# Kernel optimization log

Measured on AMD Instinct MI355X. Metric: run time of the kernel, lower is better.

## Reference

```python
import jax, jax.numpy as jnp
import numpy as np
from jax import lax

NUM_SEG = 64
EPS = 1e-12

def conv2d(x, w, b=None):
    y = lax.conv_general_dilated(x, w, (1, 1), 'SAME', dimension_numbers=('NCHW', 'OIHW', 'NCHW'))
    if b is not None:
        y = y + b[None, :, None, None]
    return y

def layer_norm_chw(x):
    # LayerNorm over (C,H,W) per sample, no affine
    mu = x.mean(axis=(1, 2, 3), keepdims=True)
    var = jnp.mean((x - mu) ** 2, axis=(1, 2, 3), keepdims=True)
    return (x - mu) / jnp.sqrt(var + EPS)

def spade(x, sem_rs, w_sh, b_sh, w_g, b_g, w_be, b_be):
    xn = layer_norm_chw(x)
    h = jax.nn.relu(conv2d(sem_rs, w_sh, b_sh))
    gamma = conv2d(h, w_g, b_g)
    beta = conv2d(h, w_be, b_be)
    return xn * (1.0 + gamma) + beta

def painted_semantic_map(f_sem, segmap):
    # f_sem: [B,C,Hp,Wp] float; segmap: [B,Hi,Wi] int
    B, C, Hp, Wp = f_sem.shape
    _, Hi, Wi = segmap.shape
    # torch nearest interpolate: src = floor(dst * in/out)
    rows = (jnp.arange(Hp) * Hi) // Hp
    cols = (jnp.arange(Wp) * Wi) // Wp
    seg_small = segmap[:, rows[:, None], cols[None, :]]  # [B,Hp,Wp]
    flat_feat = f_sem.transpose(0, 2, 3, 1).reshape(-1, C)  # [B*Hp*Wp, C]
    bidx = jnp.repeat(jnp.arange(B), Hp * Wp)
    gid = bidx * NUM_SEG + jnp.clip(seg_small.reshape(-1), 0, NUM_SEG - 1)
    sums = jax.ops.segment_sum(flat_feat, gid, num_segments=B * NUM_SEG)
    cnts = jax.ops.segment_sum(jnp.ones((flat_feat.shape[0],), flat_feat.dtype), gid, num_segments=B * NUM_SEG)
    # scatter_mean + nan_to_num: empty segments -> 0
    avg = jnp.where(cnts[:, None] > 0, sums / jnp.maximum(cnts, 1.0)[:, None], 0.0)
    pid = jnp.repeat(jnp.arange(B), Hi * Wi) * NUM_SEG + jnp.clip(segmap.reshape(-1), 0, NUM_SEG - 1)
    return avg[pid].reshape(B, Hi, Wi, C).transpose(0, 3, 1, 2)  # [B,C,Hi,Wi]

def setup_inputs() -> dict:
    key = jax.random.key(0)
    ks = jax.random.split(key, 32)
    B, Cm, Cs, Hp, Wp, Hi, Wi, Hm = 2, 1536, 384, 32, 32, 448, 448, 128
    d = {}
    d['x_main'] = jax.random.normal(ks[0], (B, Cm, Hp, Wp), jnp.float32)
    d['f_semantic'] = jax.random.normal(ks[1], (B, Cs, Hp, Wp), jnp.float32)
    s = 0.02
    d['w_sh0'] = jax.random.normal(ks[2], (Hm, Cs, 3, 3), jnp.float32) * s
    d['b_sh0'] = jax.random.normal(ks[3], (Hm,), jnp.float32) * s
    d['w_g0'] = jax.random.normal(ks[4], (Cm, Hm, 3, 3), jnp.float32) * s
    d['b_g0'] = jax.random.normal(ks[5], (Cm,), jnp.float32) * s
    d['w_be0'] = jax.random.normal(ks[6], (Cm, Hm, 3, 3), jnp.float32) * s
    d['b_be0'] = jax.random.normal(ks[7], (Cm,), jnp.float32) * s
    d['w_sh1'] = jax.random.normal(ks[8], (Hm, Cs, 3, 3), jnp.float32) * s
    d['b_sh1'] = jax.random.normal(ks[9], (Hm,), jnp.float32) * s
    d['w_g1'] = jax.random.normal(ks[10], (8, Hm, 3, 3), jnp.float32) * s
    d['b_g1'] = jax.random.normal(ks[11], (8,), jnp.float32) * s
    d['w_be1'] = jax.random.normal(ks[12], (8, Hm, 3, 3), jnp.float32) * s
    d['b_be1'] = jax.random.normal(ks[13], (8,), jnp.float32) * s
    d['w_sh2'] = jax.random.normal(ks[14], (Hm, Cs, 3, 3), jnp.float32) * s
    d['b_sh2'] = jax.random.normal(ks[15], (Hm,), jnp.float32) * s
    d['w_g2'] = jax.random.normal(ks[16], (16, Hm, 3, 3), jnp.float32) * s
    d['b_g2'] = jax.random.normal(ks[17], (16,), jnp.float32) * s
    d['w_be2'] = jax.random.normal(ks[18], (16, Hm, 3, 3), jnp.float32) * s
    d['b_be2'] = jax.random.normal(ks[19], (16,), jnp.float32) * s
    d['w_c0'] = jax.random.normal(ks[20], (8, Cm, 1, 1), jnp.float32) * s
    d['bias0'] = jax.random.normal(ks[21], (8,), jnp.float32) * s
    d['w_c1'] = jax.random.normal(ks[22], (16, 8, 1, 1), jnp.float32) * s
    d['bias1'] = jax.random.normal(ks[23], (16,), jnp.float32) * s
    d['w_c2'] = jax.random.normal(ks[24], (1, 16, 1, 1), jnp.float32) * s
    d['bias2'] = jax.random.normal(ks[25], (1,), jnp.float32) * s
    d['segmap'] = jax.random.randint(ks[26], (B, Hi, Wi), 0, NUM_SEG, jnp.int32)
    return d

def reference(x_main, f_semantic, w_sh0, b_sh0, w_g0, b_g0, w_be0, b_be0,
              w_sh1, b_sh1, w_g1, b_g1, w_be1, b_be1,
              w_sh2, b_sh2, w_g2, b_g2, w_be2, b_be2,
              w_c0, bias0, w_c1, bias1, w_c2, bias2, segmap):
    B, Cm, Hp, Wp = x_main.shape
    pm = painted_semantic_map(f_semantic, segmap)  # [B,Cs,Hi,Wi]
    # bilinear (align_corners=False) resize to main-path resolution; identical at all 3 SPADE layers
    sem_rs = jax.image.resize(pm, (B, pm.shape[1], Hp, Wp), method='bilinear')
    h = spade(x_main, sem_rs, w_sh0, b_sh0, w_g0, b_g0, w_be0, b_be0)
    h = jax.nn.softplus(conv2d(h, w_c0) + bias0[None, :, None, None])
    h = spade(h, sem_rs, w_sh1, b_sh1, w_g1, b_g1, w_be1, b_be1)
    h = jax.nn.softplus(conv2d(h, w_c1) + bias1[None, :, None, None])
    h = spade(h, sem_rs, w_sh2, b_sh2, w_g2, b_g2, w_be2, b_be2)
    h = jax.nn.softplus(conv2d(h, w_c2) + bias2[None, :, None, None])
    return h
```

## Files before the change

kernel.cpp:

```cpp
#include <hip/hip_runtime.h>
#include <hip/hip_bf16.h>

#define DEV __device__ __forceinline__

constexpr int B = 2;
constexpr int CM = 1536;
constexpr int CS = 384;
constexpr int HP = 32, WP = 32, P = 1024;
constexpr int HI = 448, WI = 448;
constexpr int HM = 128;
constexpr int NSEG = 64;

constexpr size_t OFF_AVG  = 0;
constexpr size_t OFF_SEMT = 49152;
constexpr size_t OFF_HSHT = 835584;
constexpr size_t OFF_OUT0 = 1622016;
constexpr size_t OFF_P6   = 4767744;
constexpr size_t OFF_H1A  = 5160960;
constexpr size_t OFF_OUT1 = 5177344;
constexpr size_t OFF_H2A  = 5193728;
constexpr size_t OFF_OUT2 = 5226496;
constexpr size_t OFF_STATS= 5259264;
constexpr size_t OFF_PACK = 5259280;

constexpr size_t PK0 = 0;
constexpr size_t PK1 = 1327104;
constexpr size_t PK2 = 4866048;
constexpr size_t PK3 = 4902912;
constexpr int    PK_CHUNKS = 617472;

typedef __attribute__((ext_vector_type(8))) short s16x8;
typedef __attribute__((ext_vector_type(4))) float f32x4;

DEV float softplus_f(float x) {
    return fmaxf(x, 0.f) + log1pf(expf(-fabsf(x)));
}
DEV ushort f2bf(float f) {
    union { float f; unsigned u; } x; x.f = f;
    unsigned r = x.u + 0x7fffu + ((x.u >> 16) & 1u);
    return (ushort)(r >> 16);
}
DEV float bf2f(ushort u) {
    union { unsigned u; float f; } x; x.u = ((unsigned)u) << 16;
    return x.f;
}

__global__ __launch_bounds__(256) void k_seg_avg(const float* __restrict__ f_sem,
                                                 const int* __restrict__ segmap,
                                                 float* __restrict__ ws) {
    int b = blockIdx.y;
    int c0 = blockIdx.x * 8;
    __shared__ int   segs[P];
    __shared__ float sums[NSEG][9];
    __shared__ float cnt[NSEG];
    int t = threadIdx.x;
    for (int i = t; i < NSEG * 9; i += 256) (&sums[0][0])[i] = 0.f;
    if (t < NSEG) cnt[t] = 0.f;
    __syncthreads();
    for (int p = t; p < P; p += 256) {
        int i = p >> 5, j = p & 31;
        int s = segmap[(b * HI + i * 14) * WI + j * 14];
        s = min(max(s, 0), NSEG - 1);
        segs[p] = s;
        atomicAdd(&cnt[s], 1.f);
    }
    __syncthreads();
    #pragma unroll
    for (int ch = 0; ch < 8; ++ch) {
        const float* fp = f_sem + ((size_t)b * CS + c0 + ch) * P;
        #pragma unroll
        for (int pb = 0; pb < 4; ++pb) {
            int p = pb * 256 + t;
            float v = fp[p];
            atomicAdd(&sums[segs[p]][ch], v);
        }
    }
    __syncthreads();
    for (int i = t; i < NSEG * 8; i += 256) {
        int s = i >> 3, ch = i & 7;
        float cv = cnt[s];
        ws[OFF_AVG + ((size_t)(b * NSEG + s)) * CS + c0 + ch] =
            cv > 0.f ? sums[s][ch] / cv : 0.f;
    }
}

__global__ __launch_bounds__(256) void k_paint(const int* __restrict__ segmap,
                                               float* __restrict__ ws) {
    int oxt = blockIdx.x, oy = blockIdx.y, b = blockIdx.z;
    int ox0 = oxt * 8;
    __shared__ float WbT[8][65];
    __shared__ float norm[8];
    int t = threadIdx.x;
    for (int i = t; i < 8 * 65; i += 256) (&WbT[0][0])[i] = 0.f;
    __syncthreads();

    float cy = 14.f * oy + 6.5f;
    int y0 = 14 * oy - 7;
    int x0 = 14 * ox0 - 7;
    for (int k = t; k < 28 * 126; k += 256) {
        int r = k / 126, cix = k % 126;
        int jy = y0 + r, jx = x0 + cix;
        if (jy < 0 || jy >= HI || jx < 0 || jx >= WI) continue;
        float wy = 1.f - fabsf(cy - (float)jy) * (1.f / 14.f);
        int s = segmap[(b * HI + jy) * WI + jx];
        s = min(max(s, 0), NSEG - 1);
        int oxhi = (jx + 7) / 14;
        #pragma unroll
        for (int d = 0; d < 2; ++d) {
            int ox = oxhi - d;
            if (ox < ox0 || ox >= ox0 + 8) continue;
            float wx = 1.f - fabsf(14.f * ox + 6.5f - (float)jx) * (1.f / 14.f);
            if (wx > 0.f) atomicAdd(&WbT[ox - ox0][s], wy * wx);
        }
    }
    __syncthreads();
    if (t < 8) {
        float sm = 0.f;
        #pragma unroll
        for (int s = 0; s < NSEG; ++s) sm += WbT[t][s];
        norm[t] = 1.f / sm;
    }
    __syncthreads();

    const float* ap0 = ws + OFF_AVG + (size_t)b * NSEG * CS;
    for (int c = t; c < CS; c += 256) {
        float acc[8] = {};
        const float* ap = ap0 + c;
        #pragma unroll
        for (int s = 0; s < NSEG; ++s) {
            float a = ap[(size_t)s * CS];
            #pragma unroll
            for (int ox = 0; ox < 8; ++ox) acc[ox] += WbT[ox][s] * a;
        }
        #pragma unroll
        for (int ox = 0; ox < 8; ++ox) {
            int op = oy * 32 + ox0 + ox;
            ws[OFF_SEMT + ((size_t)b * P + op) * CS + c] = acc[ox] * norm[ox];
        }
    }
}

__global__ __launch_bounds__(256) void k_ln0_stats(const float* __restrict__ x,
                                                   float* __restrict__ stats) {
    int b = blockIdx.y;
    const float4* xp = (const float4*)(x + (size_t)b * CM * P);
    int n4 = CM * P / 4;
    float s = 0.f, q = 0.f;
    for (int i = blockIdx.x * 256 + threadIdx.x; i < n4; i += 64 * 256) {
        float4 v = xp[i];
        s += v.x + v.y + v.z + v.w;
        q += v.x * v.x + v.y * v.y + v.z * v.z + v.w * v.w;
    }
    for (int o = 32; o > 0; o >>= 1) { s += __shfl_down(s, o); q += __shfl_down(q, o); }
    __shared__ float ls[4], lq[4];
    int w = threadIdx.x >> 6;
    if ((threadIdx.x & 63) == 0) { ls[w] = s; lq[w] = q; }
    __syncthreads();
    if (threadIdx.x == 0) {
        atomicAdd(&stats[b * 2],     ls[0] + ls[1] + ls[2] + ls[3]);
        atomicAdd(&stats[b * 2 + 1], lq[0] + lq[1] + lq[2] + lq[3]);
    }
}

__global__ __launch_bounds__(256) void k_wpack(
    const float* __restrict__ w_sh0, const float* __restrict__ w_sh1, const float* __restrict__ w_sh2,
    const float* __restrict__ w_g0,  const float* __restrict__ w_be0,
    const float* __restrict__ w_g1,  const float* __restrict__ w_be1,
    const float* __restrict__ w_g2,  const float* __restrict__ w_be2,
    ushort* __restrict__ packU)
{
    for (int c8 = blockIdx.x * 256 + threadIdx.x; c8 < PK_CHUNKS; c8 += gridDim.x * 256) {
        size_t e = (size_t)c8 * 8;
        const float* s0 = nullptr;
        bool zero = false;
        if (e < PK1) {
            size_t r = e;
            int ci0 = (int)(r & 31), co2 = (int)((r >> 5) & 31);
            int tap = (int)((r >> 10) % 9);
            int kct = (int)((r / 9216) % 12), ct = (int)(r / 110592);
            int coG = ct * 32 + co2, sel = coG >> 7, cow = coG & 127;
            const float* wp = sel == 0 ? w_sh0 : (sel == 1 ? w_sh1 : w_sh2);
            s0 = &wp[((size_t)cow * CS + kct * 32 + ci0) * 9 + tap];
        } else if (e < PK2) {
            size_t r = e - PK1;
            int ci0 = (int)(r & 31), co2 = (int)((r >> 5) & 31);
            int tap = (int)((r >> 10) % 9);
            int kct = (int)((r / 9216) % 4), ct = (int)(r / 36864);
            int cog = ct * 16 + (co2 & 15);
            const float* wp = co2 < 16 ? w_g0 : w_be0;
            s0 = &wp[((size_t)cog * HM + kct * 32 + ci0) * 9 + tap];
        } else if (e < PK3) {
            size_t r = e - PK2;
            int ci0 = (int)(r & 31), co2 = (int)((r >> 5) & 31);
            int tap = (int)((r >> 10) % 9);
            int kct = (int)(r / 9216);
            zero = ((co2 & 15) >= 8);
            int cog = co2 & 7;
            const float* wp = co2 < 16 ? w_g1 : w_be1;
            if (!zero) s0 = &wp[((size_t)cog * HM + kct * 32 + ci0) * 9 + tap];
        } else {
            size_t r = e - PK3;
            int ci0 = (int)(r & 31), co2 = (int)((r >> 5) & 31);
            int tap = (int)((r >> 10) % 9);
            int kct = (int)(r / 9216);
            int cog = co2 & 15;
            const float* wp = co2 < 16 ? w_g2 : w_be2;
            s0 = &wp[((size_t)cog * HM + kct * 32 + ci0) * 9 + tap];
        }
        s16x8 o;
        #pragma unroll
        for (int i = 0; i < 8; ++i) {
            float v = zero ? 0.f : s0[(size_t)i * 9];
            o[i] = (short)f2bf(v);
        }
        *(s16x8*)&packU[e] = o;
    }
}

template<int MODE>
__global__ __launch_bounds__(256) void k_conv_mfma(
    const float* __restrict__ semT, const ushort* __restrict__ hshTin,
    const ushort* __restrict__ packW,
    const float* __restrict__ bb0, const float* __restrict__ bb1,
    const float* __restrict__ xsrc, const float* __restrict__ st, float Ninv,
    const float* __restrict__ wcf, const float* __restrict__ bcf,
    float* __restrict__ fout, float* __restrict__ statsOut,
    ushort* __restrict__ outH)
{
    constexpr int ROWS = (MODE == 0) ? 4 : 8;
    constexpr int NT   = ROWS / 2;
    constexpr int XR   = ROWS + 2;
    constexpr int KTOT = (MODE == 0) ? 12 : 4;
    constexpr int CBASE = (MODE == 2) ? 128 : (MODE == 3) ? 256 : 0;
    constexpr int NP = (MODE == 1) ? 1536 : (MODE == 2) ? 8 : 16;

    int pt = blockIdx.x, ctile = blockIdx.y;
    int zz = blockIdx.z;
    int b  = (MODE == 0) ? (zz % B) : zz;
    int ks = (MODE == 0) ? (zz / B) : 0;
    int t = threadIdx.x, l = t & 63, wv = t >> 6;
    int y0 = pt * ROWS;

    __shared__ __align__(16) ushort Wl[9][32][40];
    __shared__ __align__(16) ushort Xl[XR][34][40];

    f32x4 acc[2][NT] = {};

    for (int kc = 0; kc < 128; kc += 32) {
        __syncthreads();
        for (int j = t; j < XR * 34 * 4; j += 256) {
            int slot = j >> 2, part = j & 3;
            int r = slot / 34, c = slot % 34;
            int gy = y0 - 1 + r, gx = c - 1;
            s16x8 v = {};
            if (gy >= 0 && gy < HP && gx >= 0 && gx < WP) {
                int pix = gy * WP + gx;
                if constexpr (MODE == 0) {
                    const float4* sp = (const float4*)&semT[((size_t)b * P + pix) * CS + ks * 128 + kc + part * 8];
                    float4 x0 = sp[0], x1 = sp[1];
                    v[0] = (short)f2bf(x0.x); v[1] = (short)f2bf(x0.y);
                    v[2] = (short)f2bf(x0.z); v[3] = (short)f2bf(x0.w);
                    v[4] = (short)f2bf(x1.x); v[5] = (short)f2bf(x1.y);
                    v[6] = (short)f2bf(x1.z); v[7] = (short)f2bf(x1.w);
                } else {
                    v = *(const s16x8*)&hshTin[((size_t)b * P + pix) * 384 + CBASE + kc + part * 8];
                }
            }
            *(s16x8*)&Xl[r][c][part * 8] = v;
        }
        const ushort* wsrc = packW + (size_t)(ctile * KTOT + ks * 4 + (kc >> 5)) * 9216;
        for (int j = t; j < 1152; j += 256) {
            int tap = j >> 7, co2 = (j >> 2) & 31, part = j & 3;
            *(s16x8*)&Wl[tap][co2][part * 8] = *(const s16x8*)&wsrc[(size_t)j * 8];
        }
        __syncthreads();
        #pragma unroll
        for (int tap = 0; tap < 9; ++tap) {
            int dy = tap / 3, dx = tap % 3;
            s16x8 a0 = *(const s16x8*)&Wl[tap][l & 15][(l >> 4) * 8];
            s16x8 a1 = *(const s16x8*)&Wl[tap][16 + (l & 15)][(l >> 4) * 8];
            #pragma unroll
            for (int nt = 0; nt < NT; ++nt) {
                int q = wv * (16 * NT) + nt * 16 + (l & 15);
                int ry = (q >> 5) + dy, rx = (q & 31) + dx;
                s16x8 bf = *(const s16x8*)&Xl[ry][rx][(l >> 4) * 8];
                acc[0][nt] = __builtin_amdgcn_mfma_f32_16x16x32_bf16(a0, bf, acc[0][nt], 0, 0, 0);
                acc[1][nt] = __builtin_amdgcn_mfma_f32_16x16x32_bf16(a1, bf, acc[1][nt], 0, 0, 0);
            }
        }
    }

    if constexpr (MODE == 0) {
        __syncthreads();
        ushort (*T)[36] = (ushort(*)[36])(&Xl[0][0][0]);
        #pragma unroll
        for (int mt = 0; mt < 2; ++mt)
            #pragma unroll
            for (int nt = 0; nt < NT; ++nt)
                #pragma unroll
                for (int r = 0; r < 4; ++r) {
                    int m = mt * 16 + (l >> 4) * 4 + r;
                    int pl = wv * (16 * NT) + nt * 16 + (l & 15);
                    T[pl][m] = f2bf(acc[mt][nt][r]);
                }
        __syncthreads();
        int row = t >> 1, half = t & 1;
        ushort* dst = outH + ((size_t)((ks * B + b) * P) + pt * 128 + row) * 384 + ctile * 32 + half * 16;
        *(s16x8*)dst = *(const s16x8*)&T[row][half * 16];
    } else if constexpr (MODE == 1) {
        float mu = st[b * 2] * Ninv;
        float var = st[b * 2 + 1] * Ninv - mu * mu;
        float rs = rsqrtf(var + 1e-12f);
        __syncthreads();
        float (*WC)[17] = (float(*)[17])(&Wl[0][0][0]);
        if (t < 128) WC[t >> 4][t & 15] = wcf[(size_t)(t >> 4) * CM + ctile * 16 + (t & 15)];
        __syncthreads();
        float pacc[8][4] = {};
        #pragma unroll
        for (int nt = 0; nt < NT; ++nt)
            #pragma unroll
            for (int r = 0; r < 4; ++r) {
                int m = (l >> 4) * 4 + r;
                int cog = ctile * 16 + m;
                int px = pt * 256 + wv * 64 + nt * 16 + (l & 15);
                float gam = acc[0][nt][r] + bb0[cog];
                float bet = acc[1][nt][r] + bb1[cog];
                float xv = xsrc[((size_t)b * NP + cog) * P + px];
                float o0 = (xv - mu) * rs * (1.f + gam) + bet;
                #pragma unroll
                for (int o = 0; o < 8; ++o) pacc[o][nt] += WC[o][m] * o0;
            }
        #pragma unroll
        for (int o = 0; o < 8; ++o)
            #pragma unroll
            for (int nt = 0; nt < NT; ++nt) {
                float v = pacc[o][nt];
                v += __shfl_xor(v, 16);
                v += __shfl_xor(v, 32);
                if ((l >> 4) == 0)
                    fout[(((size_t)b * 96 + ctile) * 8 + o) * P + pt * 256 + wv * 64 + nt * 16 + l] = v;
            }
    } else if constexpr (MODE == 2) {
        float mu = st[b * 2] * Ninv;
        float var = st[b * 2 + 1] * Ninv - mu * mu;
        float rs = rsqrtf(var + 1e-12f);
        __syncthreads();
        float (*O1)[9] = (float(*)[9])(&Xl[0][0][0]);
        #pragma unroll
        for (int nt = 0; nt < NT; ++nt)
            #pragma unroll
            for (int r = 0; r < 4; ++r) {
                int m = (l >> 4) * 4 + r;
                if (m < 8) {
                    int pxl = wv * 64 + nt * 16 + (l & 15);
                    int px = pt * 256 + pxl;
                    float gam = acc[0][nt][r] + bb0[m];
                    float bet = acc[1][nt][r] + bb1[m];
                    float xv = xsrc[((size_t)b * NP + m) * P + px];
                    O1[pxl][m] = (xv - mu) * rs * (1.f + gam) + bet;
                }
            }
        __syncthreads();
        float vin[8];
        #pragma unroll
        for (int ci = 0; ci < 8; ++ci) vin[ci] = O1[t][ci];
        float s = 0.f, q = 0.f;
        #pragma unroll
        for (int o = 0; o < 16; ++o) {
            float a = bcf[o];
            #pragma unroll
            for (int ci = 0; ci < 8; ++ci) a += wcf[o * 8 + ci] * vin[ci];
            a = softplus_f(a);
            fout[((size_t)b * 16 + o) * P + pt * 256 + t] = a;
            s += a; q += a * a;
        }
        for (int o2 = 32; o2 > 0; o2 >>= 1) { s += __shfl_down(s, o2); q += __shfl_down(q, o2); }
        float* red = (float*)&Wl[0][0][0];
        if ((t & 63) == 0) { red[wv] = s; red[4 + wv] = q; }
        __syncthreads();
        if (t == 0) {
            atomicAdd(&statsOut[b * 2],     red[0] + red[1] + red[2] + red[3]);
            atomicAdd(&statsOut[b * 2 + 1], red[4] + red[5] + red[6] + red[7]);
        }
    } else {
        float mu = st[b * 2] * Ninv;
        float var = st[b * 2 + 1] * Ninv - mu * mu;
        float rs = rsqrtf(var + 1e-12f);
        __syncthreads();
        float (*O2)[17] = (float(*)[17])(&Xl[0][0][0]);
        #pragma unroll
        for (int nt = 0; nt < NT; ++nt)
            #pragma unroll
            for (int r = 0; r < 4; ++r) {
                int m = (l >> 4) * 4 + r;
                int pxl = wv * 64 + nt * 16 + (l & 15);
                int px = pt * 256 + pxl;
                float gam = acc[0][nt][r] + bb0[m];
                float bet = acc[1][nt][r] + bb1[m];
                float xv = xsrc[((size_t)b * NP + m) * P + px];
                O2[pxl][m] = (xv - mu) * rs * (1.f + gam) + bet;
            }
        __syncthreads();
        float a = bcf[0];
        #pragma unroll
        for (int ci = 0; ci < 16; ++ci) a += wcf[ci] * O2[t][ci];
        fout[(size_t)b * P + pt * 256 + t] = softplus_f(a);
    }
}

__global__ __launch_bounds__(256) void k_hsh_fin(const ushort* __restrict__ part,
                                                 const float* __restrict__ b0,
                                                 const float* __restrict__ b1,
                                                 const float* __restrict__ b2,
                                                 ushort* __restrict__ hsh) {
    int gid = blockIdx.x * 256 + threadIdx.x;
    int grp = gid % 48, pixg = gid / 48;
    int ch0 = grp * 8;
    size_t base = (size_t)pixg * 384 + ch0;
    s16x8 p0 = *(const s16x8*)&part[(size_t)0 * B * P * 384 + base];
    s16x8 p1 = *(const s16x8*)&part[(size_t)1 * B * P * 384 + base];
    s16x8 p2 = *(const s16x8*)&part[(size_t)2 * B * P * 384 + base];
    int sel = ch0 >> 7;
    const float* bp = sel == 0 ? b0 : (sel == 1 ? b1 : b2);
    int cb = ch0 & 127;
    s16x8 o;
    #pragma unroll
    for (int i = 0; i < 8; ++i) {
        float v = bf2f((ushort)p0[i]) + bf2f((ushort)p1[i]) + bf2f((ushort)p2[i]) + bp[cb + i];
        o[i] = (short)f2bf(fmaxf(v, 0.f));
    }
    *(s16x8*)&hsh[base] = o;
}

__global__ __launch_bounds__(256) void k_c1a_fin(const float* __restrict__ part,
                                                 const float* __restrict__ bias,
                                                 float* __restrict__ h1a,
                                                 float* __restrict__ stats) {
    int b = blockIdx.y, t = threadIdx.x;
    int idx = blockIdx.x * 256 + t;
    int o = idx >> 10, pix = idx & 1023;
    float v = 0.f;
    #pragma unroll 8
    for (int ct = 0; ct < 96; ++ct)
        v += part[(((size_t)b * 96 + ct) * 8 + o) * P + pix];
    v += bias[o];
    v = softplus_f(v);
    h1a[((size_t)b * 8 + o) * P + pix] = v;
    float s = v, q = v * v;
    for (int o2 = 32; o2 > 0; o2 >>= 1) { s += __shfl_down(s, o2); q += __shfl_down(q, o2); }
    __shared__ float ls[4], lq[4];
    int w = t >> 6;
    if ((t & 63) == 0) { ls[w] = s; lq[w] = q; }
    __syncthreads();
    if (t == 0) {
        atomicAdd(&stats[(B + b) * 2],     ls[0] + ls[1] + ls[2] + ls[3]);
        atomicAdd(&stats[(B + b) * 2 + 1], lq[0] + lq[1] + lq[2] + lq[3]);
    }
}

extern "C" void kernel_launch(void* const* d_in, const int* in_sizes, int n_in,
                              void* d_out, int out_size, void* d_ws, size_t ws_size,
                              hipStream_t stream) {
    const float* x_main = (const float*)d_in[0];
    const float* f_sem  = (const float*)d_in[1];
    const float* w_sh0 = (const float*)d_in[2];  const float* b_sh0 = (const float*)d_in[3];
    const float* w_g0  = (const float*)d_in[4];  const float* b_g0  = (const float*)d_in[5];
    const float* w_be0 = (const float*)d_in[6];  const float* b_be0 = (const float*)d_in[7];
    const float* w_sh1 = (const float*)d_in[8];  const float* b_sh1 = (const float*)d_in[9];
    const float* w_g1  = (const float*)d_in[10]; const float* b_g1  = (const float*)d_in[11];
    const float* w_be1 = (const float*)d_in[12]; const float* b_be1 = (const float*)d_in[13];
    const float* w_sh2 = (const float*)d_in[14]; const float* b_sh2 = (const float*)d_in[15];
    const float* w_g2  = (const float*)d_in[16]; const float* b_g2  = (const float*)d_in[17];
    const float* w_be2 = (const float*)d_in[18]; const float* b_be2 = (const float*)d_in[19];
    const float* w_c0  = (const float*)d_in[20]; const float* bias0 = (const float*)d_in[21];
    const float* w_c1  = (const float*)d_in[22]; const float* bias1 = (const float*)d_in[23];
    const float* w_c2  = (const float*)d_in[24]; const float* bias2 = (const float*)d_in[25];
    const int*   segmap = (const int*)d_in[26];

    float* ws = (float*)d_ws;
    float* out = (float*)d_out;
    float* stats = ws + OFF_STATS;
    ushort* hshU = (ushort*)(ws + OFF_HSHT);
    ushort* partU = (ushort*)(ws + OFF_OUT0);
    float*  partA = ws + OFF_OUT0;
    ushort* packU = (ushort*)(ws + OFF_PACK);

    hipMemsetAsync((void*)stats, 0, 16 * sizeof(float), stream);

    k_wpack<<<dim3(2412), 256, 0, stream>>>(w_sh0, w_sh1, w_sh2, w_g0, w_be0,
                                            w_g1, w_be1, w_g2, w_be2, packU);
    k_seg_avg<<<dim3(48, B), 256, 0, stream>>>(f_sem, segmap, ws);
    k_ln0_stats<<<dim3(64, B), 256, 0, stream>>>(x_main, stats);
    k_paint<<<dim3(4, 32, B), 256, 0, stream>>>(segmap, ws);

    k_conv_mfma<0><<<dim3(8, 12, 3 * B), 256, 0, stream>>>(
        ws + OFF_SEMT, nullptr, packU + PK0,
        nullptr, nullptr, nullptr, nullptr, 0.f,
        nullptr, nullptr, nullptr, nullptr, partU);
    k_hsh_fin<<<dim3(384), 256, 0, stream>>>(partU, b_sh0, b_sh1, b_sh2, hshU);

    k_conv_mfma<1><<<dim3(4, 96, B), 256, 0, stream>>>(
        nullptr, hshU, packU + PK1,
        b_g0, b_be0, x_main, stats, 1.f / (float)(CM * P),
        w_c0, nullptr, partA, nullptr, nullptr);
    k_c1a_fin<<<dim3(32, B), 256, 0, stream>>>(partA, bias0, ws + OFF_H1A, stats);

    k_conv_mfma<2><<<dim3(4, 1, B), 256, 0, stream>>>(
        nullptr, hshU, packU + PK2,
        b_g1, b_be1, ws + OFF_H1A, stats + 2 * B, 1.f / (float)(8 * P),
        w_c1, bias1, ws + OFF_H2A, stats + 4 * B, nullptr);

    k_conv_mfma<3><<<dim3(4, 1, B), 256, 0, stream>>>(
        nullptr, hshU, packU + PK3,
        b_g2, b_be2, ws + OFF_H2A, stats + 4 * B, 1.f / (float)(16 * P),
        w_c2, bias2, out, nullptr, nullptr);
}
```

Measured before the change: 306.4 us.

## Split paint into weight-table and GEMV kernels, emit bf16, coalesce weight packing

```diff
diff --git a/kernel.cpp b/kernel.cpp
--- a/kernel.cpp
+++ b/kernel.cpp
@@ -15,11 +15,9 @@
 constexpr size_t OFF_SEMT = 49152;
 constexpr size_t OFF_HSHT = 835584;
 constexpr size_t OFF_OUT0 = 1622016;
-constexpr size_t OFF_P6   = 4767744;
+constexpr size_t OFF_WTBL = 4767744;
 constexpr size_t OFF_H1A  = 5160960;
-constexpr size_t OFF_OUT1 = 5177344;
 constexpr size_t OFF_H2A  = 5193728;
-constexpr size_t OFF_OUT2 = 5226496;
 constexpr size_t OFF_STATS= 5259264;
 constexpr size_t OFF_PACK = 5259280;
 
@@ -27,7 +25,6 @@
 constexpr size_t PK1 = 1327104;
 constexpr size_t PK2 = 4866048;
 constexpr size_t PK3 = 4902912;
-constexpr int    PK_CHUNKS = 617472;
 
 typedef __attribute__((ext_vector_type(8))) short s16x8;
 typedef __attribute__((ext_vector_type(4))) float f32x4;
@@ -84,8 +81,8 @@
     }
 }
 
-__global__ __launch_bounds__(256) void k_paint(const int* __restrict__ segmap,
-                                               float* __restrict__ ws) {
+__global__ __launch_bounds__(256) void k_paint_w(const int* __restrict__ segmap,
+                                                 float* __restrict__ Wt) {
     int oxt = blockIdx.x, oy = blockIdx.y, b = blockIdx.z;
     int ox0 = oxt * 8;
     __shared__ float WbT[8][65];
@@ -121,22 +118,41 @@
         norm[t] = 1.f / sm;
     }
     __syncthreads();
-
-    const float* ap0 = ws + OFF_AVG + (size_t)b * NSEG * CS;
-    for (int c = t; c < CS; c += 256) {
-        float acc[8] = {};
-        const float* ap = ap0 + c;
-        #pragma unroll
-        for (int s = 0; s < NSEG; ++s) {
-            float a = ap[(size_t)s * CS];
-            #pragma unroll
-            for (int ox = 0; ox < 8; ++ox) acc[ox] += WbT[ox][s] * a;
-        }
-        #pragma unroll
-        for (int ox = 0; ox < 8; ++ox) {
-            int op = oy * 32 + ox0 + ox;
-            ws[OFF_SEMT + ((size_t)b * P + op) * CS + c] = acc[ox] * norm[ox];
-        }
+    for (int i = t; i < 8 * 64; i += 256) {
+        int ox = i >> 6, s = i & 63;
+        int op = oy * 32 + ox0 + ox;
+        Wt[((size_t)b * P + op) * 64 + s] = WbT[ox][s] * norm[ox];
+    }
+}
+
+__global__ __launch_bounds__(256) void k_paint_gemv(const float* __restrict__ Wt,
+                                                    const float* __restrict__ avg,
+                                                    ushort* __restrict__ semB) {
+    int pt = blockIdx.x, ctb = blockIdx.y, b = blockIdx.z;
+    __shared__ float WL[32][65];
+    __shared__ float AL[64][33];
+    int t = threadIdx.x;
+    for (int i = t; i < 2048; i += 256) {
+        int p = i >> 6, s = i & 63;
+        WL[p][s] = Wt[((size_t)b * P + pt * 32 + p) * 64 + s];
+    }
+    for (int i = t; i < 2048; i += 256) {
+        int s = i >> 5, c = i & 31;
+        AL[s][c] = avg[((size_t)b * NSEG + s) * CS + ctb * 32 + c];
+    }
+    __syncthreads();
+    int c = t & 31, pg = t >> 5;
+    float acc[4] = {};
+    #pragma unroll 16
+    for (int s = 0; s < 64; ++s) {
+        float a = AL[s][c];
+        #pragma unroll
+        for (int k = 0; k < 4; ++k) acc[k] += WL[pg + 8 * k][s] * a;
+    }
+    #pragma unroll
+    for (int k = 0; k < 4; ++k) {
+        int pix = pt * 32 + pg + 8 * k;
+        semB[((size_t)b * P + pix) * 384 + ctb * 32 + c] = f2bf(acc[k]);
     }
 }
 
@@ -169,57 +185,61 @@
     const float* __restrict__ w_g2,  const float* __restrict__ w_be2,
     ushort* __restrict__ packU)
 {
-    for (int c8 = blockIdx.x * 256 + threadIdx.x; c8 < PK_CHUNKS; c8 += gridDim.x * 256) {
-        size_t e = (size_t)c8 * 8;
-        const float* s0 = nullptr;
-        bool zero = false;
-        if (e < PK1) {
-            size_t r = e;
-            int ci0 = (int)(r & 31), co2 = (int)((r >> 5) & 31);
-            int tap = (int)((r >> 10) % 9);
-            int kct = (int)((r / 9216) % 12), ct = (int)(r / 110592);
+    int sl = blockIdx.x;
+    __shared__ float buf[32][289];
+    __shared__ const float* sp[32];
+    __shared__ size_t pbase_s;
+    int t = threadIdx.x;
+    if (t < 32) {
+        int co2 = t;
+        const float* p = nullptr;
+        size_t pbase;
+        if (sl < 144) {
+            int ct = sl / 12, kct = sl % 12;
             int coG = ct * 32 + co2, sel = coG >> 7, cow = coG & 127;
             const float* wp = sel == 0 ? w_sh0 : (sel == 1 ? w_sh1 : w_sh2);
-            s0 = &wp[((size_t)cow * CS + kct * 32 + ci0) * 9 + tap];
-        } else if (e < PK2) {
-            size_t r = e - PK1;
-            int ci0 = (int)(r & 31), co2 = (int)((r >> 5) & 31);
-            int tap = (int)((r >> 10) % 9);
-            int kct = (int)((r / 9216) % 4), ct = (int)(r / 36864);
+            p = wp + ((size_t)cow * CS + kct * 32) * 9;
+            pbase = PK0 + (size_t)sl * 9216;
+        } else if (sl < 528) {
+            int s2 = sl - 144;
+            int ct = s2 / 4, kct = s2 % 4;
             int cog = ct * 16 + (co2 & 15);
             const float* wp = co2 < 16 ? w_g0 : w_be0;
-            s0 = &wp[((size_t)cog * HM + kct * 32 + ci0) * 9 + tap];
-        } else if (e < PK3) {
-            size_t r = e - PK2;
-            int ci0 = (int)(r & 31), co2 = (int)((r >> 5) & 31);
-            int tap = (int)((r >> 10) % 9);
-            int kct = (int)(r / 9216);
-            zero = ((co2 & 15) >= 8);
+            p = wp + ((size_t)cog * HM + kct * 32) * 9;
+            pbase = PK1 + (size_t)s2 * 9216;
+        } else if (sl < 532) {
+            int kct = sl - 528;
             int cog = co2 & 7;
             const float* wp = co2 < 16 ? w_g1 : w_be1;
-            if (!zero) s0 = &wp[((size_t)cog * HM + kct * 32 + ci0) * 9 + tap];
+            p = ((co2 & 15) >= 8) ? nullptr : wp + ((size_t)cog * HM + kct * 32) * 9;
+            pbase = PK2 + (size_t)kct * 9216;
         } else {
-            size_t r = e - PK3;
-            int ci0 = (int)(r & 31), co2 = (int)((r >> 5) & 31);
-            int tap = (int)((r >> 10) % 9);
-            int kct = (int)(r / 9216);
+            int kct = sl - 532;
             int cog = co2 & 15;
             const float* wp = co2 < 16 ? w_g2 : w_be2;
-            s0 = &wp[((size_t)cog * HM + kct * 32 + ci0) * 9 + tap];
-        }
-        s16x8 o;
-        #pragma unroll
-        for (int i = 0; i < 8; ++i) {
-            float v = zero ? 0.f : s0[(size_t)i * 9];
-            o[i] = (short)f2bf(v);
-        }
-        *(s16x8*)&packU[e] = o;
+            p = wp + ((size_t)cog * HM + kct * 32) * 9;
+            pbase = PK3 + (size_t)kct * 9216;
+        }
+        sp[co2] = p;
+        if (t == 0) pbase_s = pbase;
+    }
+    __syncthreads();
+    for (int j = t; j < 9216; j += 256) {
+        int co2 = j / 288, idx = j % 288;
+        const float* p = sp[co2];
+        buf[co2][idx] = p ? p[idx] : 0.f;
+    }
+    __syncthreads();
+    size_t pbase = pbase_s;
+    for (int j = t; j < 9216; j += 256) {
+        int tap = j >> 10, co2 = (j >> 5) & 31, ci = j & 31;
+        packU[pbase + j] = f2bf(buf[co2][ci * 9 + tap]);
     }
 }
 
 template<int MODE>
 __global__ __launch_bounds__(256) void k_conv_mfma(
-    const float* __restrict__ semT, const ushort* __restrict__ hshTin,
+    const ushort* __restrict__ hshTin,
     const ushort* __restrict__ packW,
     const float* __restrict__ bb0, const float* __restrict__ bb1,
     const float* __restrict__ xsrc, const float* __restrict__ st, float Ninv,
@@ -255,16 +275,8 @@
             s16x8 v = {};
             if (gy >= 0 && gy < HP && gx >= 0 && gx < WP) {
                 int pix = gy * WP + gx;
-                if constexpr (MODE == 0) {
-                    const float4* sp = (const float4*)&semT[((size_t)b * P + pix) * CS + ks * 128 + kc + part * 8];
-                    float4 x0 = sp[0], x1 = sp[1];
-                    v[0] = (short)f2bf(x0.x); v[1] = (short)f2bf(x0.y);
-                    v[2] = (short)f2bf(x0.z); v[3] = (short)f2bf(x0.w);
-                    v[4] = (short)f2bf(x1.x); v[5] = (short)f2bf(x1.y);
-                    v[6] = (short)f2bf(x1.z); v[7] = (short)f2bf(x1.w);
-                } else {
-                    v = *(const s16x8*)&hshTin[((size_t)b * P + pix) * 384 + CBASE + kc + part * 8];
-                }
+                v = *(const s16x8*)&hshTin[((size_t)b * P + pix) * 384 + CBASE
+                                           + (MODE == 0 ? ks * 128 : 0) + kc + part * 8];
             }
             *(s16x8*)&Xl[r][c][part * 8] = v;
         }
@@ -480,38 +492,41 @@
     float* ws = (float*)d_ws;
     float* out = (float*)d_out;
     float* stats = ws + OFF_STATS;
+    ushort* semB = (ushort*)(ws + OFF_SEMT);
     ushort* hshU = (ushort*)(ws + OFF_HSHT);
     ushort* partU = (ushort*)(ws + OFF_OUT0);
     float*  partA = ws + OFF_OUT0;
+    float*  Wtbl  = ws + OFF_WTBL;
     ushort* packU = (ushort*)(ws + OFF_PACK);
 
     hipMemsetAsync((void*)stats, 0, 16 * sizeof(float), stream);
 
-    k_wpack<<<dim3(2412), 256, 0, stream>>>(w_sh0, w_sh1, w_sh2, w_g0, w_be0,
-                                            w_g1, w_be1, w_g2, w_be2, packU);
+    k_wpack<<<dim3(536), 256, 0, stream>>>(w_sh0, w_sh1, w_sh2, w_g0, w_be0,
+                                           w_g1, w_be1, w_g2, w_be2, packU);
     k_seg_avg<<<dim3(48, B), 256, 0, stream>>>(f_sem, segmap, ws);
     k_ln0_stats<<<dim3(64, B), 256, 0, stream>>>(x_main, stats);
-    k_paint<<<dim3(4, 32, B), 256, 0, stream>>>(segmap, ws);
+    k_paint_w<<<dim3(4, 32, B), 256, 0, stream>>>(segmap, Wtbl);
+    k_paint_gemv<<<dim3(32, 12, B), 256, 0, stream>>>(Wtbl, ws + OFF_AVG, semB);
 
     k_conv_mfma<0><<<dim3(8, 12, 3 * B), 256, 0, stream>>>(
-        ws + OFF_SEMT, nullptr, packU + PK0,
+        semB, packU + PK0,
         nullptr, nullptr, nullptr, nullptr, 0.f,
         nullptr, nullptr, nullptr, nullptr, partU);
     k_hsh_fin<<<dim3(384), 256, 0, stream>>>(partU, b_sh0, b_sh1, b_sh2, hshU);
 
     k_conv_mfma<1><<<dim3(4, 96, B), 256, 0, stream>>>(
-        nullptr, hshU, packU + PK1,
+        hshU, packU + PK1,
         b_g0, b_be0, x_main, stats, 1.f / (float)(CM * P),
         w_c0, nullptr, partA, nullptr, nullptr);
     k_c1a_fin<<<dim3(32, B), 256, 0, stream>>>(partA, bias0, ws + OFF_H1A, stats);
 
     k_conv_mfma<2><<<dim3(4, 1, B), 256, 0, stream>>>(
-        nullptr, hshU, packU + PK2,
+        hshU, packU + PK2,
         b_g1, b_be1, ws + OFF_H1A, stats + 2 * B, 1.f / (float)(8 * P),
         w_c1, bias1, ws + OFF_H2A, stats + 4 * B, nullptr);
 
     k_conv_mfma<3><<<dim3(4, 1, B), 256, 0, stream>>>(
-        nullptr, hshU, packU + PK3,
+        hshU, packU + PK3,
         b_g2, b_be2, ws + OFF_H2A, stats + 4 * B, 1.f / (float)(16 * P),
         w_c2, bias2, out, nullptr, nullptr);
 }
```

Measured after the change: 282.5 us. 7.8% less time.
